# Performance work log

Measured on AMD Instinct MI355X. Metric: run time of the kernel, lower is better.

The kernel has to match this reference:

```python
import jax, jax.numpy as jnp
import numpy as np

N = 8192
D_IN = 128
D_OUT = 128


def setup_inputs() -> dict:
    key = jax.random.key(0)
    k1, k2, k3, k4 = jax.random.split(key, 4)
    x = jax.random.normal(k1, (N, D_IN), dtype=jnp.float32)
    adj = jax.random.uniform(k2, (N, N), dtype=jnp.float32)
    # nn.Linear params: weight [out, in], bias [out]
    bound = 1.0 / np.sqrt(D_IN)
    W = jax.random.uniform(k3, (D_OUT, D_IN), minval=-bound, maxval=bound, dtype=jnp.float32)
    b = jax.random.uniform(k4, (D_OUT,), minval=-bound, maxval=bound, dtype=jnp.float32)
    return {"x": x, "adj": adj, "W": W, "b": b}


def reference(x, adj, W, b):
    # Symmetric normalization: D^{-1/2} A D^{-1/2}, expressed as fused
    # row/col scaling instead of materializing diagonal matrices.
    rowsum = adj.sum(axis=1)                      # [N]
    d_inv_sqrt = jnp.power(rowsum, -0.5)
    d_inv_sqrt = jnp.where(jnp.isinf(d_inv_sqrt), 0.0, d_inv_sqrt)
    adj_norm = d_inv_sqrt[:, None] * adj * d_inv_sqrt[None, :]  # [N, N]
    h = adj_norm @ x                              # [N, D_IN]
    return h @ W.T + b                            # [N, D_OUT]
```

## Files before the change

kernel.cpp:

```cpp
#include <hip/hip_runtime.h>
#include <hip/hip_bf16.h>

typedef short bf16x8 __attribute__((ext_vector_type(8)));
typedef float f32x16 __attribute__((ext_vector_type(16)));

#define GN 8192
#define GD 128


__global__ __launch_bounds__(256) void k_rowsum(const float* __restrict__ adj,
                                                float* __restrict__ s) {
  const int row = blockIdx.x;
  const float4* p = (const float4*)(adj + (size_t)row * GN);
  float acc = 0.f;
#pragma unroll
  for (int i = 0; i < 8; ++i) {
    float4 v = p[threadIdx.x + i * 256];
    acc += (v.x + v.y) + (v.z + v.w);
  }
#pragma unroll
  for (int off = 32; off > 0; off >>= 1) acc += __shfl_down(acc, off, 64);
  __shared__ float red[4];
  if ((threadIdx.x & 63) == 0) red[threadIdx.x >> 6] = acc;
  __syncthreads();
  if (threadIdx.x == 0) {
    float t = (red[0] + red[1]) + (red[2] + red[3]);
    s[row] = (t > 0.f) ? rsqrtf(t) : 0.f;
  }
}

__global__ __launch_bounds__(256) void k_pack(const float* __restrict__ x,
                                              const float* __restrict__ s,
                                              __hip_bfloat16* __restrict__ xsp) {
  const int kb = blockIdx.x;
  const int t = threadIdx.x;
  __shared__ float tile[64][129];
  __shared__ float sv[64];
  if (t < 64) sv[t] = s[kb * 64 + t];
  __syncthreads();
  const float4* xp = (const float4*)(x + (size_t)kb * 64 * GD);
#pragma unroll
  for (int j = 0; j < 8; ++j) {
    int i = t + j * 256;
    int r = i >> 5, c4 = i & 31;
    float4 v = xp[i];
    float sc = sv[r];
    tile[r][c4 * 4 + 0] = v.x * sc;
    tile[r][c4 * 4 + 1] = v.y * sc;
    tile[r][c4 * 4 + 2] = v.z * sc;
    tile[r][c4 * 4 + 3] = v.w * sc;
  }
  __syncthreads();
  const int c = t >> 1, h = t & 1;
  __hip_bfloat16 buf[32];
#pragma unroll
  for (int kk = 0; kk < 32; ++kk) buf[kk] = __float2bfloat16(tile[h * 32 + kk][c]);
  __hip_bfloat16* op = xsp + (size_t)kb * (128 * 72) + c * 72 + h * 32;
#pragma unroll
  for (int j = 0; j < 4; ++j) ((uint4*)op)[j] = ((uint4*)buf)[j];
}

__global__ __launch_bounds__(256, 2) void k_gemm(const float* __restrict__ adj,
                                                 const __hip_bfloat16* __restrict__ xsp,
                                                 float* __restrict__ part) {
  __shared__ __align__(16) __hip_bfloat16 Asm[64 * 72];
  __shared__ __align__(16) __hip_bfloat16 Bsm[128 * 72];
  const int mb = blockIdx.x;
  const int ks = blockIdx.y;
  const int t = threadIdx.x;
  const int lane = t & 63;
  const int wave = t >> 6;
  const int wm = wave >> 1, wn = wave & 1;

  f32x16 acc0, acc1;
#pragma unroll
  for (int i = 0; i < 16; ++i) { acc0[i] = 0.f; acc1[i] = 0.f; }

  const int ar = t >> 2;
  const int acg = (t & 3) * 16;
  const float* arow = adj + (size_t)(mb * 64 + ar) * GN + (size_t)ks * 2048 + acg;
  const uint4* bsrc_base = (const uint4*)(xsp + (size_t)(ks * 32) * (128 * 72));

  const int a_lds_off = ar * 72 + acg;
  const int afrag_row = wm * 32 + (lane & 31);
  const int koff = (lane >> 5) * 8;
  const int bcol0 = wn * 64 + (lane & 31);

  for (int kt = 0; kt < 32; ++kt) {
    float v[16];
    const float4* s4 = (const float4*)(arow + (size_t)kt * 64);
#pragma unroll
    for (int j = 0; j < 4; ++j) {
      float4 q = s4[j];
      v[j * 4 + 0] = q.x; v[j * 4 + 1] = q.y; v[j * 4 + 2] = q.z; v[j * 4 + 3] = q.w;
    }
    {
      __hip_bfloat16 hb[16];
#pragma unroll
      for (int i = 0; i < 16; ++i) hb[i] = __float2bfloat16(v[i]);
      uint4* d = (uint4*)(Asm + a_lds_off);
      d[0] = ((uint4*)hb)[0];
      d[1] = ((uint4*)hb)[1];
    }
    {
      const uint4* bsv = bsrc_base + (size_t)kt * 1152;
      uint4* bd = (uint4*)Bsm;
      for (int i = t; i < 1152; i += 256) bd[i] = bsv[i];
    }
    __syncthreads();
#pragma unroll
    for (int kk = 0; kk < 64; kk += 16) {
      bf16x8 af = *(const bf16x8*)(Asm + afrag_row * 72 + kk + koff);
      bf16x8 b0 = *(const bf16x8*)(Bsm + bcol0 * 72 + kk + koff);
      bf16x8 b1 = *(const bf16x8*)(Bsm + (bcol0 + 32) * 72 + kk + koff);
      acc0 = __builtin_amdgcn_mfma_f32_32x32x16_bf16(af, b0, acc0, 0, 0, 0);
      acc1 = __builtin_amdgcn_mfma_f32_32x32x16_bf16(af, b1, acc1, 0, 0, 0);
    }
    __syncthreads();
  }

  float* pb = part + (size_t)ks * GN * GD + (size_t)(mb * 64 + wm * 32) * GD + wn * 64;
#pragma unroll
  for (int reg = 0; reg < 16; ++reg) {
    int r = (reg & 3) + 8 * (reg >> 2) + 4 * (lane >> 5);
    int cc = lane & 31;
    pb[(size_t)r * GD + cc] = acc0[reg];
    pb[(size_t)r * GD + cc + 32] = acc1[reg];
  }
}

__global__ __launch_bounds__(256) void k_out(const float* __restrict__ part,
                                             const float* __restrict__ s,
                                             const float* __restrict__ W,
                                             const float* __restrict__ b,
                                             float* __restrict__ out) {
  __shared__ __align__(16) __hip_bfloat16 Hs[32 * 136];
  __shared__ __align__(16) __hip_bfloat16 Ws[128 * 136];
  __shared__ float bs[128];
  const int t = threadIdx.x;
  const int rowbase = blockIdx.x * 32;
  if (t < 128) bs[t] = b[t];
#pragma unroll
  for (int j = 0; j < 4; ++j) {
    int i = t + j * 256;
    int r = i >> 5, c4 = i & 31;
    size_t idx = (size_t)(rowbase + r) * GD + c4 * 4;
    float4 p0 = *(const float4*)(part + idx);
    float4 p1 = *(const float4*)(part + idx + (size_t)GN * GD);
    float4 p2 = *(const float4*)(part + idx + (size_t)2 * GN * GD);
    float4 p3 = *(const float4*)(part + idx + (size_t)3 * GN * GD);
    float sc = s[rowbase + r];
    __hip_bfloat16 hb[4];
    hb[0] = __float2bfloat16((p0.x + p1.x + p2.x + p3.x) * sc);
    hb[1] = __float2bfloat16((p0.y + p1.y + p2.y + p3.y) * sc);
    hb[2] = __float2bfloat16((p0.z + p1.z + p2.z + p3.z) * sc);
    hb[3] = __float2bfloat16((p0.w + p1.w + p2.w + p3.w) * sc);
    *(uint2*)(Hs + r * 136 + c4 * 4) = *(uint2*)hb;
  }
#pragma unroll
  for (int j = 0; j < 16; ++j) {
    int i = t + j * 256;
    int o = i >> 5, k4 = i & 31;
    float4 w = *(const float4*)(W + (size_t)o * GD + k4 * 4);
    __hip_bfloat16 hb[4];
    hb[0] = __float2bfloat16(w.x);
    hb[1] = __float2bfloat16(w.y);
    hb[2] = __float2bfloat16(w.z);
    hb[3] = __float2bfloat16(w.w);
    *(uint2*)(Ws + o * 136 + k4 * 4) = *(uint2*)hb;
  }
  __syncthreads();
  const int lane = t & 63;
  const int wave = t >> 6;
  const int arow = lane & 31;
  const int koff = (lane >> 5) * 8;
  const int bcol = wave * 32 + (lane & 31);
  f32x16 acc;
#pragma unroll
  for (int i = 0; i < 16; ++i) acc[i] = 0.f;
#pragma unroll
  for (int kk = 0; kk < 128; kk += 16) {
    bf16x8 af = *(const bf16x8*)(Hs + arow * 136 + kk + koff);
    bf16x8 bf = *(const bf16x8*)(Ws + bcol * 136 + kk + koff);
    acc = __builtin_amdgcn_mfma_f32_32x32x16_bf16(af, bf, acc, 0, 0, 0);
  }
#pragma unroll
  for (int reg = 0; reg < 16; ++reg) {
    int r = (reg & 3) + 8 * (reg >> 2) + 4 * (lane >> 5);
    out[(size_t)(rowbase + r) * GD + bcol] = acc[reg] + bs[bcol];
  }
}

extern "C" void kernel_launch(void* const* d_in, const int* in_sizes, int n_in,
                              void* d_out, int out_size, void* d_ws, size_t ws_size,
                              hipStream_t stream) {
  const float* x   = (const float*)d_in[0];
  const float* adj = (const float*)d_in[1];
  const float* W   = (const float*)d_in[2];
  const float* b   = (const float*)d_in[3];
  float* out = (float*)d_out;

  float* s = (float*)d_ws;
  __hip_bfloat16* xsp = (__hip_bfloat16*)((char*)d_ws + 32768);
  float* part = (float*)((char*)d_ws + 32768 + 128 * 128 * 144);

  k_rowsum<<<8192, 256, 0, stream>>>(adj, s);
  k_pack<<<128, 256, 0, stream>>>(x, s, xsp);
  k_gemm<<<dim3(128, 4), 256, 0, stream>>>(adj, xsp, part);
  k_out<<<256, 256, 0, stream>>>(part, s, W, b, out);
}
```

Baseline: 455.9 us.

## Fuse row-scaling and bf16 conversion of adj into rowsum pass, widen split-K

```diff
diff --git a/kernel.cpp b/kernel.cpp
--- a/kernel.cpp
+++ b/kernel.cpp
@@ -3,29 +3,49 @@
 
 typedef short bf16x8 __attribute__((ext_vector_type(8)));
 typedef float f32x16 __attribute__((ext_vector_type(16)));
+typedef float f32x4v __attribute__((ext_vector_type(4)));
 
 #define GN 8192
 #define GD 128
-
-
-__global__ __launch_bounds__(256) void k_rowsum(const float* __restrict__ adj,
-                                                float* __restrict__ s) {
+#define KSPLIT 8
+
+
+__global__ __launch_bounds__(256) void k_rowcvt(const float* __restrict__ adj,
+                                                float* __restrict__ s,
+                                                __hip_bfloat16* __restrict__ adjb) {
   const int row = blockIdx.x;
-  const float4* p = (const float4*)(adj + (size_t)row * GN);
+  const int t = threadIdx.x;
+  const f32x4v* p = (const f32x4v*)(adj + (size_t)row * GN);
+  f32x4v v[8];
   float acc = 0.f;
 #pragma unroll
   for (int i = 0; i < 8; ++i) {
-    float4 v = p[threadIdx.x + i * 256];
-    acc += (v.x + v.y) + (v.z + v.w);
+    v[i] = __builtin_nontemporal_load(p + t + i * 256);
+    acc += (v[i].x + v[i].y) + (v[i].z + v[i].w);
   }
 #pragma unroll
   for (int off = 32; off > 0; off >>= 1) acc += __shfl_down(acc, off, 64);
   __shared__ float red[4];
-  if ((threadIdx.x & 63) == 0) red[threadIdx.x >> 6] = acc;
-  __syncthreads();
-  if (threadIdx.x == 0) {
-    float t = (red[0] + red[1]) + (red[2] + red[3]);
-    s[row] = (t > 0.f) ? rsqrtf(t) : 0.f;
+  __shared__ float sbc;
+  if ((t & 63) == 0) red[t >> 6] = acc;
+  __syncthreads();
+  if (t == 0) {
+    float tot = (red[0] + red[1]) + (red[2] + red[3]);
+    float sc = (tot > 0.f) ? rsqrtf(tot) : 0.f;
+    sbc = sc;
+    s[row] = sc;
+  }
+  __syncthreads();
+  const float sc = sbc;
+  __hip_bfloat16* orow = adjb + (size_t)row * GN;
+#pragma unroll
+  for (int i = 0; i < 8; ++i) {
+    __hip_bfloat16 hb[4];
+    hb[0] = __float2bfloat16(v[i].x * sc);
+    hb[1] = __float2bfloat16(v[i].y * sc);
+    hb[2] = __float2bfloat16(v[i].z * sc);
+    hb[3] = __float2bfloat16(v[i].w * sc);
+    *(uint2*)(orow + (size_t)(t + i * 256) * 4) = *(uint2*)hb;
   }
 }
 
@@ -60,7 +80,7 @@
   for (int j = 0; j < 4; ++j) ((uint4*)op)[j] = ((uint4*)buf)[j];
 }
 
-__global__ __launch_bounds__(256, 2) void k_gemm(const float* __restrict__ adj,
+__global__ __launch_bounds__(256, 4) void k_gemm(const __hip_bfloat16* __restrict__ adjb,
                                                  const __hip_bfloat16* __restrict__ xsp,
                                                  float* __restrict__ part) {
   __shared__ __align__(16) __hip_bfloat16 Asm[64 * 72];
@@ -78,29 +98,22 @@
 
   const int ar = t >> 2;
   const int acg = (t & 3) * 16;
-  const float* arow = adj + (size_t)(mb * 64 + ar) * GN + (size_t)ks * 2048 + acg;
-  const uint4* bsrc_base = (const uint4*)(xsp + (size_t)(ks * 32) * (128 * 72));
+  const __hip_bfloat16* arow = adjb + (size_t)(mb * 64 + ar) * GN + ks * 1024 + acg;
+  const uint4* bsrc_base = (const uint4*)(xsp + (size_t)(ks * 16) * (128 * 72));
 
   const int a_lds_off = ar * 72 + acg;
   const int afrag_row = wm * 32 + (lane & 31);
   const int koff = (lane >> 5) * 8;
   const int bcol0 = wn * 64 + (lane & 31);
 
-  for (int kt = 0; kt < 32; ++kt) {
-    float v[16];
-    const float4* s4 = (const float4*)(arow + (size_t)kt * 64);
-#pragma unroll
-    for (int j = 0; j < 4; ++j) {
-      float4 q = s4[j];
-      v[j * 4 + 0] = q.x; v[j * 4 + 1] = q.y; v[j * 4 + 2] = q.z; v[j * 4 + 3] = q.w;
-    }
+  for (int kt = 0; kt < 16; ++kt) {
     {
-      __hip_bfloat16 hb[16];
-#pragma unroll
-      for (int i = 0; i < 16; ++i) hb[i] = __float2bfloat16(v[i]);
+      const uint4* s4 = (const uint4*)(arow + (size_t)kt * 64);
+      uint4 q0 = s4[0];
+      uint4 q1 = s4[1];
       uint4* d = (uint4*)(Asm + a_lds_off);
-      d[0] = ((uint4*)hb)[0];
-      d[1] = ((uint4*)hb)[1];
+      d[0] = q0;
+      d[1] = q1;
     }
     {
       const uint4* bsv = bsrc_base + (size_t)kt * 1152;
@@ -130,7 +143,6 @@
 }
 
 __global__ __launch_bounds__(256) void k_out(const float* __restrict__ part,
-                                             const float* __restrict__ s,
                                              const float* __restrict__ W,
                                              const float* __restrict__ b,
                                              float* __restrict__ out) {
@@ -145,16 +157,17 @@
     int i = t + j * 256;
     int r = i >> 5, c4 = i & 31;
     size_t idx = (size_t)(rowbase + r) * GD + c4 * 4;
-    float4 p0 = *(const float4*)(part + idx);
-    float4 p1 = *(const float4*)(part + idx + (size_t)GN * GD);
-    float4 p2 = *(const float4*)(part + idx + (size_t)2 * GN * GD);
-    float4 p3 = *(const float4*)(part + idx + (size_t)3 * GN * GD);
-    float sc = s[rowbase + r];
+    float4 a = {0.f, 0.f, 0.f, 0.f};
+#pragma unroll
+    for (int ksl = 0; ksl < KSPLIT; ++ksl) {
+      float4 p = *(const float4*)(part + idx + (size_t)ksl * GN * GD);
+      a.x += p.x; a.y += p.y; a.z += p.z; a.w += p.w;
+    }
     __hip_bfloat16 hb[4];
-    hb[0] = __float2bfloat16((p0.x + p1.x + p2.x + p3.x) * sc);
-    hb[1] = __float2bfloat16((p0.y + p1.y + p2.y + p3.y) * sc);
-    hb[2] = __float2bfloat16((p0.z + p1.z + p2.z + p3.z) * sc);
-    hb[3] = __float2bfloat16((p0.w + p1.w + p2.w + p3.w) * sc);
+    hb[0] = __float2bfloat16(a.x);
+    hb[1] = __float2bfloat16(a.y);
+    hb[2] = __float2bfloat16(a.z);
+    hb[3] = __float2bfloat16(a.w);
     *(uint2*)(Hs + r * 136 + c4 * 4) = *(uint2*)hb;
   }
 #pragma unroll
@@ -201,11 +214,12 @@
   float* out = (float*)d_out;
 
   float* s = (float*)d_ws;
-  __hip_bfloat16* xsp = (__hip_bfloat16*)((char*)d_ws + 32768);
-  float* part = (float*)((char*)d_ws + 32768 + 128 * 128 * 144);
-
-  k_rowsum<<<8192, 256, 0, stream>>>(adj, s);
+  __hip_bfloat16* xsp  = (__hip_bfloat16*)((char*)d_ws + 32768);
+  __hip_bfloat16* adjb = (__hip_bfloat16*)((char*)d_ws + 2392064);
+  float* part = (float*)((char*)d_ws + 136609792);
+
+  k_rowcvt<<<8192, 256, 0, stream>>>(adj, s, adjb);
   k_pack<<<128, 256, 0, stream>>>(x, s, xsp);
-  k_gemm<<<dim3(128, 4), 256, 0, stream>>>(adj, xsp, part);
-  k_out<<<256, 256, 0, stream>>>(part, s, W, b, out);
-}
+  k_gemm<<<dim3(128, KSPLIT), 256, 0, stream>>>(adjb, xsp, part);
+  k_out<<<256, 256, 0, stream>>>(part, W, b, out);
+}
```

After: 414.1 us. -9.2%, faster.
